# Kernel tuning notes

Measured on AMD Instinct MI355X. Metric: run time of the kernel, lower is better.

## Reference

```python
import jax, jax.numpy as jnp
import numpy as np

B, L, D = 4096, 50, 64
NU, NI, NR = 100000, 100000, 5


def setup_inputs() -> dict:
    key = jax.random.key(0)
    ks = jax.random.split(key, 16)
    s = 0.02
    inp = {
        "nodes_v": jax.random.randint(ks[0], (B,), 0, NI),
        "neigh_u": jax.random.randint(ks[1], (B, L), 0, NU),
        "neigh_r": jax.random.randint(ks[2], (B, L), 0, NR),
        "embed_u": jax.random.normal(ks[3], (NU, D)) * s,
        "embed_i": jax.random.normal(ks[4], (NI, D)) * s,
        "embed_r": jax.random.normal(ks[5], (NR, D)) * s,
        # gv MLP: Linear(2D,D) ReLU Linear(D,D) ReLU Linear(D,D)
        "gv_w1": jax.random.normal(ks[6], (2 * D, D)) * s, "gv_b1": jnp.zeros((D,)),
        "gv_w2": jax.random.normal(ks[7], (D, D)) * s,     "gv_b2": jnp.zeros((D,)),
        "gv_w3": jax.random.normal(ks[8], (D, D)) * s,     "gv_b3": jnp.zeros((D,)),
        # attention MLP: Linear(2D,D) ReLU Linear(D,D) ReLU Linear(D,1), softmax over neighbors
        "att_w1": jax.random.normal(ks[9], (2 * D, D)) * s, "att_b1": jnp.zeros((D,)),
        "att_w2": jax.random.normal(ks[10], (D, D)) * s,    "att_b2": jnp.zeros((D,)),
        "att_w3": jax.random.normal(ks[11], (D, 1)) * s,    "att_b3": jnp.zeros((1,)),
        # combine: Linear(2D,D) ReLU Linear(D,D) ReLU
        "wr1_w": jax.random.normal(ks[12], (2 * D, D)) * s, "wr1_b": jnp.zeros((D,)),
        "wr2_w": jax.random.normal(ks[13], (D, D)) * s,     "wr2_b": jnp.zeros((D,)),
    }
    return inp


def reference(nodes_v, neigh_u, neigh_r, embed_u, embed_i, embed_r,
              gv_w1, gv_b1, gv_w2, gv_b2, gv_w3, gv_b3,
              att_w1, att_b1, att_w2, att_b2, att_w3, att_b3,
              wr1_w, wr1_b, wr2_w, wr2_b):
    qj = embed_i[nodes_v]            # [B, D] item reps
    pt = embed_u[neigh_u]            # [B, L, D] neighbor user reps
    er = embed_r[neigh_r]            # [B, L, D] rating reps
    # fusion MLP g(.)
    x = jnp.concatenate([pt, er], axis=-1)                    # [B, L, 2D]
    h = jax.nn.relu(x @ gv_w1 + gv_b1)
    h = jax.nn.relu(h @ gv_w2 + gv_b2)
    fjt = h @ gv_w3 + gv_b3                                   # [B, L, D]
    # attention over neighbors (dropout is identity in eval mode)
    q_rep = jnp.broadcast_to(qj[:, None, :], fjt.shape)       # [B, L, D]
    a = jnp.concatenate([fjt, q_rep], axis=-1)                # [B, L, 2D]
    a = jax.nn.relu(a @ att_w1 + att_b1)
    a = jax.nn.relu(a @ att_w2 + att_b2)
    scores = (a @ att_w3 + att_b3)[..., 0]                    # [B, L]
    mu = jax.nn.softmax(scores, axis=1)                       # softmax over neighbors
    zj = jnp.einsum("bld,bl->bd", fjt, mu)                   # weighted aggregation
    # combine aggregated neighborhood with item's own embedding (2D -> D)
    z = jax.nn.relu(jnp.concatenate([zj, qj], axis=-1) @ wr1_w + wr1_b)
    out = jax.nn.relu(z @ wr2_w + wr2_b)                      # [B, D]
    return out
```

## Files before the change

kernel.cpp:

```cpp
#include <hip/hip_runtime.h>

typedef __bf16 bf16;
typedef short s16x8 __attribute__((ext_vector_type(8)));
typedef __bf16 b16x8 __attribute__((ext_vector_type(8)));
typedef float f32x4 __attribute__((ext_vector_type(4)));

#define B_   4096
#define L_   50
#define SH   72

#define OFF_W1F  0
#define OFF_W2F  8192
#define OFF_W3F  12288
#define OFF_WCF  16384
#define OFF_A2F  20480
#define OFF_R1T  24576
#define OFF_R2T  32768
#define WT_TOTAL 36864
#define BIAS1P_BYTE 73728
#define CQ_BYTE     73984
#define EU16_BYTE   1122560
#define ER16_BYTE   13922560
#define WS_NEED     13923200

#define PREP_W_BLOCKS 145
#define CQ_BLOCKS     32
#define CONV_THREADS  800040
#define CONV_BLOCKS   3126

__device__ __forceinline__ unsigned short f2b(float f) {
    __bf16 h = (__bf16)f;
    return __builtin_bit_cast(unsigned short, h);
}
__device__ __forceinline__ unsigned pack2(float a, float b) {
    return (unsigned)f2b(a) | ((unsigned)f2b(b) << 16);
}
__device__ __forceinline__ s16x8 mkfrag(float4 a, float4 b) {
    union { s16x8 v; unsigned u[4]; } r;
    r.u[0] = pack2(a.x, a.y); r.u[1] = pack2(a.z, a.w);
    r.u[2] = pack2(b.x, b.y); r.u[3] = pack2(b.z, b.w);
    return r.v;
}
__device__ __forceinline__ f32x4 mfma16(s16x8 a, s16x8 b, f32x4 c) {
    return __builtin_amdgcn_mfma_f32_16x16x32_bf16(a, b, c, 0, 0, 0);
}

extern "C" __global__ void prep_all(const float* __restrict__ w1, const float* __restrict__ w2,
                                    const float* __restrict__ w3, const float* __restrict__ a1,
                                    const float* __restrict__ a2, const float* __restrict__ r1,
                                    const float* __restrict__ r2, const float* __restrict__ gb3,
                                    const float* __restrict__ ab1,
                                    const int* __restrict__ nodes_v, const float* __restrict__ embed_i,
                                    const float* __restrict__ embed_u, const float* __restrict__ embed_r,
                                    bf16* __restrict__ wt, float* __restrict__ bias1p,
                                    float* __restrict__ cq,
                                    bf16* __restrict__ eu16, bf16* __restrict__ er16)
{
    if (blockIdx.x >= PREP_W_BLOCKS + CQ_BLOCKS) {
        long t = (long)(blockIdx.x - PREP_W_BLOCKS - CQ_BLOCKS) * 256 + threadIdx.x;
        if (t < 800000) {
            const float* s = embed_u + t * 8;
            float4 a = *(const float4*)s, b = *(const float4*)(s + 4);
            *(s16x8*)(eu16 + t * 8) = mkfrag(a, b);
        } else if (t < CONV_THREADS) {
            long r = (t - 800000) * 8;
            const float* s = embed_r + r;
            float4 a = *(const float4*)s, b = *(const float4*)(s + 4);
            *(s16x8*)(er16 + r) = mkfrag(a, b);
        }
        return;
    }
    if (blockIdx.x >= PREP_W_BLOCKS) {
        int wv   = (blockIdx.x - PREP_W_BLOCKS) * 4 + (threadIdx.x >> 6);
        int lane = threadIdx.x & 63, m = lane & 15, quad = lane >> 4;
        int base = wv * 32;
        int i0 = base + m, i1 = base + 16 + m;
        int v0 = nodes_v[i0], v1 = nodes_v[i1];

        s16x8 bfr[8];
#pragma unroll
        for (int kt = 0; kt < 2; ++kt)
#pragma unroll
            for (int nt = 0; nt < 4; ++nt) {
                const float* src = a1 + (64 + kt * 32 + quad * 8) * 64 + nt * 16 + m;
                union { s16x8 v; unsigned u[4]; } fr;
#pragma unroll
                for (int jj = 0; jj < 4; ++jj)
                    fr.u[jj] = pack2(src[(2 * jj) * 64], src[(2 * jj + 1) * 64]);
                bfr[kt * 4 + nt] = fr.v;
            }

        f32x4 ac0[4] = {}, ac1[4] = {};
#pragma unroll
        for (int kt = 0; kt < 2; ++kt) {
            const float* q0 = embed_i + (size_t)v0 * 64 + kt * 32 + quad * 8;
            const float* q1 = embed_i + (size_t)v1 * 64 + kt * 32 + quad * 8;
            s16x8 aq0 = mkfrag(*(const float4*)q0, *(const float4*)(q0 + 4));
            s16x8 aq1 = mkfrag(*(const float4*)q1, *(const float4*)(q1 + 4));
#pragma unroll
            for (int nt = 0; nt < 4; ++nt) {
                ac0[nt] = mfma16(aq0, bfr[kt * 4 + nt], ac0[nt]);
                ac1[nt] = mfma16(aq1, bfr[kt * 4 + nt], ac1[nt]);
            }
        }
#pragma unroll
        for (int nt = 0; nt < 4; ++nt) {
            int c = nt * 16 + m;
#pragma unroll
            for (int r4 = 0; r4 < 4; ++r4) {
                cq[(base + quad * 4 + r4) * 64 + c]      = ac0[nt][r4];
                cq[(base + 16 + quad * 4 + r4) * 64 + c] = ac1[nt][r4];
            }
        }
        return;
    }
    int i = blockIdx.x * 256 + threadIdx.x;
    if (i >= WT_TOTAL + 64) return;
    if (i >= WT_TOTAL) {
        int n = i - WT_TOTAL;
        float s0 = ab1[n], s1 = 0.f, s2 = 0.f, s3 = 0.f;
#pragma unroll
        for (int t = 0; t < 64; t += 4) {
            s0 = fmaf(gb3[t],     a1[t * 64 + n],       s0);
            s1 = fmaf(gb3[t + 1], a1[(t + 1) * 64 + n], s1);
            s2 = fmaf(gb3[t + 2], a1[(t + 2) * 64 + n], s2);
            s3 = fmaf(gb3[t + 3], a1[(t + 3) * 64 + n], s3);
        }
        bias1p[n] = (s0 + s1) + (s2 + s3);
        return;
    }
    float val;
    if (i < OFF_R1T) {
        int off, kind;
        if      (i < OFF_W2F) { off = OFF_W1F; kind = 0; }
        else if (i < OFF_W3F) { off = OFF_W2F; kind = 1; }
        else if (i < OFF_WCF) { off = OFF_W3F; kind = 2; }
        else if (i < OFF_A2F) { off = OFF_WCF; kind = 3; }
        else                  { off = OFF_A2F; kind = 4; }
        int local = i - off;
        int f = local >> 9, lane = (local >> 3) & 63, j = local & 7;
        int kt = f >> 2, nt = f & 3, quad = lane >> 4, m = lane & 15;
        int k = kt * 32 + quad * 8 + j;
        int n = nt * 16 + m;
        if (kind == 0)      val = w1[k * 64 + n];
        else if (kind == 1) val = w2[k * 64 + n];
        else if (kind == 2) val = w3[k * 64 + n];
        else if (kind == 4) val = a2[k * 64 + n];
        else {
            float s0 = 0.f, s1 = 0.f, s2 = 0.f, s3 = 0.f;
#pragma unroll
            for (int t = 0; t < 64; t += 4) {
                float4 w = *(const float4*)(w3 + k * 64 + t);
                s0 = fmaf(w.x, a1[t * 64 + n],       s0);
                s1 = fmaf(w.y, a1[(t + 1) * 64 + n], s1);
                s2 = fmaf(w.z, a1[(t + 2) * 64 + n], s2);
                s3 = fmaf(w.w, a1[(t + 3) * 64 + n], s3);
            }
            val = (s0 + s1) + (s2 + s3);
        }
    }
    else if (i < OFF_R2T) { int li = i - OFF_R1T; int n = li >> 7, k = li & 127; val = r1[k * 64 + n]; }
    else                  { int li = i - OFF_R2T; int n = li >> 6, k = li & 63;  val = r2[k * 64 + n]; }
    wt[i] = (bf16)val;
}

template<bool BF16E>
__global__ void __launch_bounds__(256, 2)
dense_fused(const int* __restrict__ nodes_v, const int* __restrict__ neigh_u,
            const int* __restrict__ neigh_r,
            const float* __restrict__ embed_u, const float* __restrict__ embed_i,
            const float* __restrict__ embed_r,
            const float* __restrict__ gv_b1, const float* __restrict__ gv_b2,
            const float* __restrict__ gv_b3,
            const float* __restrict__ att_b2, const float* __restrict__ att_w3,
            const float* __restrict__ wr1_b, const float* __restrict__ wr2_b,
            const bf16* __restrict__ wt, const bf16* __restrict__ eu16,
            const bf16* __restrict__ er16, const float* __restrict__ cq,
            const float* __restrict__ bias1p, float* __restrict__ out)
{
    __shared__ __align__(16) bf16 H[128 * SH];
    __shared__ float zp[4 * 64];
    __shared__ float swm[4 * 2];
    __shared__ float qsh[2 * 64];

    const int tid = threadIdx.x;
    const int lane = tid & 63, wave = tid >> 6;
    const int m = lane & 15, quad = lane >> 4;
    const int b0 = blockIdx.x * 2;
    const int rw0 = wave * 32;
    const int item_w = rw0 >> 6;
    const int lbase = rw0 & 63;

    const int bw = b0 + item_w;
    const int l0 = min(lbase + m, L_ - 1);
    const int l1 = min(lbase + 16 + m, L_ - 1);
    const int u0 = neigh_u[bw * L_ + l0], u1 = neigh_u[bw * L_ + l1];
    const int v0 = neigh_r[bw * L_ + l0], v1 = neigh_r[bw * L_ + l1];

    float cs4[4];
#pragma unroll
    for (int nt = 0; nt < 4; ++nt) {
        int c = nt * 16 + m;
        cs4[nt] = cq[bw * 64 + c] + bias1p[c];
    }

    bf16* Hw = H + rw0 * SH;
    bf16* H0 = Hw;
    bf16* H1 = Hw + 16 * SH;

    {
        f32x4 ac0[4] = {}, ac1[4] = {};
        if constexpr (BF16E) {
            const bf16* p00 = eu16 + (size_t)u0 * 64;
            const bf16* p01 = eu16 + (size_t)u1 * 64;
            const bf16* p10 = er16 + v0 * 64;
            const bf16* p11 = er16 + v1 * 64;
#pragma unroll
            for (int kt = 0; kt < 4; ++kt) {
                const bf16* s0p = (kt < 2 ? p00 : p10) + (kt & 1) * 32 + quad * 8;
                const bf16* s1p = (kt < 2 ? p01 : p11) + (kt & 1) * 32 + quad * 8;
                s16x8 a0 = *(const s16x8*)s0p;
                s16x8 a1 = *(const s16x8*)s1p;
#pragma unroll
                for (int nt = 0; nt < 4; ++nt) {
                    s16x8 bfr = *(const s16x8*)(wt + OFF_W1F + (kt * 4 + nt) * 512 + lane * 8);
                    ac0[nt] = mfma16(a0, bfr, ac0[nt]);
                    ac1[nt] = mfma16(a1, bfr, ac1[nt]);
                }
            }
        } else {
            const float* b00 = embed_u + (size_t)u0 * 64;
            const float* b01 = embed_u + (size_t)u1 * 64;
            const float* b10 = embed_r + v0 * 64;
            const float* b11 = embed_r + v1 * 64;
#pragma unroll
            for (int kt = 0; kt < 4; ++kt) {
                const float* s0p = (kt < 2 ? b00 : b10) + (kt & 1) * 32 + quad * 8;
                const float* s1p = (kt < 2 ? b01 : b11) + (kt & 1) * 32 + quad * 8;
                float4 a0a = *(const float4*)s0p, a0b = *(const float4*)(s0p + 4);
                float4 a1a = *(const float4*)s1p, a1b = *(const float4*)(s1p + 4);
                s16x8 a0 = mkfrag(a0a, a0b);
                s16x8 a1 = mkfrag(a1a, a1b);
#pragma unroll
                for (int nt = 0; nt < 4; ++nt) {
                    s16x8 bfr = *(const s16x8*)(wt + OFF_W1F + (kt * 4 + nt) * 512 + lane * 8);
                    ac0[nt] = mfma16(a0, bfr, ac0[nt]);
                    ac1[nt] = mfma16(a1, bfr, ac1[nt]);
                }
            }
        }
#pragma unroll
        for (int nt = 0; nt < 4; ++nt) {
            int c = nt * 16 + m;
            float bv = gv_b1[c];
#pragma unroll
            for (int r4 = 0; r4 < 4; ++r4) {
                H0[(quad * 4 + r4) * SH + c] = (bf16)fmaxf(ac0[nt][r4] + bv, 0.f);
                H1[(quad * 4 + r4) * SH + c] = (bf16)fmaxf(ac1[nt][r4] + bv, 0.f);
            }
        }
    }

    {
        f32x4 ac0[4] = {}, ac1[4] = {};
#pragma unroll
        for (int kt = 0; kt < 2; ++kt) {
            s16x8 a0 = *(const s16x8*)(H0 + m * SH + kt * 32 + quad * 8);
            s16x8 a1 = *(const s16x8*)(H1 + m * SH + kt * 32 + quad * 8);
#pragma unroll
            for (int nt = 0; nt < 4; ++nt) {
                s16x8 bfr = *(const s16x8*)(wt + OFF_W2F + (kt * 4 + nt) * 512 + lane * 8);
                ac0[nt] = mfma16(a0, bfr, ac0[nt]);
                ac1[nt] = mfma16(a1, bfr, ac1[nt]);
            }
        }
#pragma unroll
        for (int nt = 0; nt < 4; ++nt) {
            int c = nt * 16 + m;
            float bv = gv_b2[c];
#pragma unroll
            for (int r4 = 0; r4 < 4; ++r4) {
                H0[(quad * 4 + r4) * SH + c] = (bf16)fmaxf(ac0[nt][r4] + bv, 0.f);
                H1[(quad * 4 + r4) * SH + c] = (bf16)fmaxf(ac1[nt][r4] + bv, 0.f);
            }
        }
    }

    f32x4 aF0[4] = {}, aF1[4] = {};
    {
        f32x4 aA0[4] = {}, aA1[4] = {};
#pragma unroll
        for (int kt = 0; kt < 2; ++kt) {
            s16x8 a0 = *(const s16x8*)(H0 + m * SH + kt * 32 + quad * 8);
            s16x8 a1 = *(const s16x8*)(H1 + m * SH + kt * 32 + quad * 8);
#pragma unroll
            for (int nt = 0; nt < 4; ++nt) {
                s16x8 bF = *(const s16x8*)(wt + OFF_W3F + (kt * 4 + nt) * 512 + lane * 8);
                s16x8 bA = *(const s16x8*)(wt + OFF_WCF + (kt * 4 + nt) * 512 + lane * 8);
                aF0[nt] = mfma16(a0, bF, aF0[nt]);
                aF1[nt] = mfma16(a1, bF, aF1[nt]);
                aA0[nt] = mfma16(a0, bA, aA0[nt]);
                aA1[nt] = mfma16(a1, bA, aA1[nt]);
            }
        }
#pragma unroll
        for (int nt = 0; nt < 4; ++nt) {
            int c = nt * 16 + m;
#pragma unroll
            for (int r4 = 0; r4 < 4; ++r4) {
                H0[(quad * 4 + r4) * SH + c] = (bf16)fmaxf(aA0[nt][r4] + cs4[nt], 0.f);
                H1[(quad * 4 + r4) * SH + c] = (bf16)fmaxf(aA1[nt][r4] + cs4[nt], 0.f);
            }
        }
    }

    float s0[4], s1[4];
    {
        f32x4 ac0[4] = {}, ac1[4] = {};
#pragma unroll
        for (int kt = 0; kt < 2; ++kt) {
            s16x8 a0 = *(const s16x8*)(H0 + m * SH + kt * 32 + quad * 8);
            s16x8 a1 = *(const s16x8*)(H1 + m * SH + kt * 32 + quad * 8);
#pragma unroll
            for (int nt = 0; nt < 4; ++nt) {
                s16x8 bfr = *(const s16x8*)(wt + OFF_A2F + (kt * 4 + nt) * 512 + lane * 8);
                ac0[nt] = mfma16(a0, bfr, ac0[nt]);
                ac1[nt] = mfma16(a1, bfr, ac1[nt]);
            }
        }
#pragma unroll
        for (int r4 = 0; r4 < 4; ++r4) { s0[r4] = 0.f; s1[r4] = 0.f; }
#pragma unroll
        for (int nt = 0; nt < 4; ++nt) {
            int c = nt * 16 + m;
            float b2v = att_b2[c], w3v = att_w3[c];
#pragma unroll
            for (int r4 = 0; r4 < 4; ++r4) {
                s0[r4] += fmaxf(ac0[nt][r4] + b2v, 0.f) * w3v;
                s1[r4] += fmaxf(ac1[nt][r4] + b2v, 0.f) * w3v;
            }
        }
#pragma unroll
        for (int mask = 1; mask < 16; mask <<= 1)
#pragma unroll
            for (int r4 = 0; r4 < 4; ++r4) {
                s0[r4] += __shfl_xor(s0[r4], mask);
                s1[r4] += __shfl_xor(s1[r4], mask);
            }
    }

    {
        const int r0b = lbase + quad * 4;
        float mloc = -1e30f;
#pragma unroll
        for (int r4 = 0; r4 < 4; ++r4) {
            if (r0b + r4 < L_)      mloc = fmaxf(mloc, s0[r4]);
            if (r0b + 16 + r4 < L_) mloc = fmaxf(mloc, s1[r4]);
        }
        mloc = fmaxf(mloc, __shfl_xor(mloc, 16));
        mloc = fmaxf(mloc, __shfl_xor(mloc, 32));

        float e0[4], e1[4], ssum = 0.f;
#pragma unroll
        for (int r4 = 0; r4 < 4; ++r4) {
            e0[r4] = (r0b + r4 < L_)      ? __expf(s0[r4] - mloc) : 0.f;
            e1[r4] = (r0b + 16 + r4 < L_) ? __expf(s1[r4] - mloc) : 0.f;
            ssum += e0[r4] + e1[r4];
        }
        ssum += __shfl_xor(ssum, 16);
        ssum += __shfl_xor(ssum, 32);

        float z[4] = {0.f, 0.f, 0.f, 0.f};
#pragma unroll
        for (int r4 = 0; r4 < 4; ++r4)
#pragma unroll
            for (int nt = 0; nt < 4; ++nt)
                z[nt] += aF0[nt][r4] * e0[r4] + aF1[nt][r4] * e1[r4];
#pragma unroll
        for (int nt = 0; nt < 4; ++nt) {
            z[nt] += __shfl_xor(z[nt], 16);
            z[nt] += __shfl_xor(z[nt], 32);
        }
        if (quad == 0) {
#pragma unroll
            for (int nt = 0; nt < 4; ++nt) zp[wave * 64 + nt * 16 + m] = z[nt];
        }
        if (lane == 0) { swm[wave * 2] = ssum; swm[wave * 2 + 1] = mloc; }
    }
    __syncthreads();

    if ((wave & 1) == 0) {
        const int item = wave >> 1;
        const int d = lane;
        float ma = swm[wave * 2 + 1],      mb = swm[(wave + 1) * 2 + 1];
        float sa = swm[wave * 2],          sb = swm[(wave + 1) * 2];
        float M  = fmaxf(ma, mb);
        float fa = __expf(ma - M), fb = __expf(mb - M);
        float zj = (fa * zp[wave * 64 + d] + fb * zp[(wave + 1) * 64 + d])
                 / (fa * sa + fb * sb) + gv_b3[d];

        float* zsh = zp + wave * 64;
        zsh[d] = zj;
        qsh[item * 64 + d] = embed_i[nodes_v[b0 + item] * 64 + d];

        float accz = wr1_b[d];
        const bf16* r1 = wt + OFF_R1T + d * 128;
#pragma unroll
        for (int k8 = 0; k8 < 8; ++k8) {
            b16x8 wv = *(const b16x8*)(r1 + k8 * 8);
#pragma unroll
            for (int j = 0; j < 8; ++j) accz = fmaf((float)wv[j], zsh[k8 * 8 + j], accz);
        }
#pragma unroll
        for (int k8 = 0; k8 < 8; ++k8) {
            b16x8 wv = *(const b16x8*)(r1 + 64 + k8 * 8);
#pragma unroll
            for (int j = 0; j < 8; ++j) accz = fmaf((float)wv[j], qsh[item * 64 + k8 * 8 + j], accz);
        }
        zsh[d] = fmaxf(accz, 0.f);

        float acco = wr2_b[d];
        const bf16* r2 = wt + OFF_R2T + d * 64;
#pragma unroll
        for (int k8 = 0; k8 < 8; ++k8) {
            b16x8 wv = *(const b16x8*)(r2 + k8 * 8);
#pragma unroll
            for (int j = 0; j < 8; ++j) acco = fmaf((float)wv[j], zsh[k8 * 8 + j], acco);
        }
        out[(b0 + item) * 64 + d] = fmaxf(acco, 0.f);
    }
}

extern "C" void kernel_launch(void* const* d_in, const int* in_sizes, int n_in,
                              void* d_out, int out_size, void* d_ws, size_t ws_size,
                              hipStream_t stream)
{
    const int* nodes_v = (const int*)d_in[0];
    const int* neigh_u = (const int*)d_in[1];
    const int* neigh_r = (const int*)d_in[2];
    const float* embed_u = (const float*)d_in[3];
    const float* embed_i = (const float*)d_in[4];
    const float* embed_r = (const float*)d_in[5];
    const float* gv_w1  = (const float*)d_in[6];  const float* gv_b1 = (const float*)d_in[7];
    const float* gv_w2  = (const float*)d_in[8];  const float* gv_b2 = (const float*)d_in[9];
    const float* gv_w3  = (const float*)d_in[10]; const float* gv_b3 = (const float*)d_in[11];
    const float* att_w1 = (const float*)d_in[12]; const float* att_b1 = (const float*)d_in[13];
    const float* att_w2 = (const float*)d_in[14]; const float* att_b2 = (const float*)d_in[15];
    const float* att_w3 = (const float*)d_in[16]; const float* att_b3 = (const float*)d_in[17];
    const float* wr1_w  = (const float*)d_in[18]; const float* wr1_b = (const float*)d_in[19];
    const float* wr2_w  = (const float*)d_in[20]; const float* wr2_b = (const float*)d_in[21];
    (void)att_b3;

    bf16*  wt     = (bf16*)d_ws;
    float* bias1p = (float*)((char*)d_ws + BIAS1P_BYTE);
    float* cq     = (float*)((char*)d_ws + CQ_BYTE);
    bf16*  eu16   = (bf16*)((char*)d_ws + EU16_BYTE);
    bf16*  er16   = (bf16*)((char*)d_ws + ER16_BYTE);

    const bool big = ws_size >= (size_t)WS_NEED;
    const int prep_grid = PREP_W_BLOCKS + CQ_BLOCKS + (big ? CONV_BLOCKS : 0);

    prep_all<<<prep_grid, 256, 0, stream>>>(
        gv_w1, gv_w2, gv_w3, att_w1, att_w2, wr1_w, wr2_w, gv_b3, att_b1,
        nodes_v, embed_i, embed_u, embed_r, wt, bias1p, cq, eu16, er16);

    if (big) {
        dense_fused<true><<<B_ / 2, 256, 0, stream>>>(nodes_v, neigh_u, neigh_r,
                                                      embed_u, embed_i, embed_r,
                                                      gv_b1, gv_b2, gv_b3, att_b2, att_w3,
                                                      wr1_b, wr2_b, wt, eu16, er16,
                                                      cq, bias1p, (float*)d_out);
    } else {
        dense_fused<false><<<B_ / 2, 256, 0, stream>>>(nodes_v, neigh_u, neigh_r,
                                                       embed_u, embed_i, embed_r,
                                                       gv_b1, gv_b2, gv_b3, att_b2, att_w3,
                                                       wr1_b, wr2_b, wt, eu16, er16,
                                                       cq, bias1p, (float*)d_out);
    }
}
```

Before: 159.3 us.

## Stage MLP weights in LDS, process four item pairs per block with gather prefetch

The fused kernel becomes persistent-ish: each block handles four item pairs instead of one. It copies the MFMA weight fragments into LDS once per block with global_load_lds, then reads them from LDS instead of global memory. The embedding gathers for the next pair are issued during the current pair's compute, with nontemporal loads to hide gather latency. In exchange it uses 48KB more LDS, which may reduce occupancy. It also launches only 512 blocks, which cuts parallelism on a 256-CU part.

```diff
diff --git a/kernel.cpp b/kernel.cpp
--- a/kernel.cpp
+++ b/kernel.cpp
@@ -17,6 +17,7 @@
 #define OFF_R1T  24576
 #define OFF_R2T  32768
 #define WT_TOTAL 36864
+#define WL_ELEMS 24576
 #define BIAS1P_BYTE 73728
 #define CQ_BYTE     73984
 #define EU16_BYTE   1122560
@@ -28,6 +29,9 @@
 #define CONV_THREADS  800040
 #define CONV_BLOCKS   3126
 
+#define DENSE_BLOCKS  512
+#define PAIRS_PER_BLK 4
+
 __device__ __forceinline__ unsigned short f2b(float f) {
     __bf16 h = (__bf16)f;
     return __builtin_bit_cast(unsigned short, h);
@@ -43,6 +47,9 @@
 }
 __device__ __forceinline__ f32x4 mfma16(s16x8 a, s16x8 b, f32x4 c) {
     return __builtin_amdgcn_mfma_f32_16x16x32_bf16(a, b, c, 0, 0, 0);
+}
+__device__ __forceinline__ s16x8 ntload16(const bf16* p) {
+    return __builtin_nontemporal_load((const s16x8*)p);
 }
 
 extern "C" __global__ void prep_all(const float* __restrict__ w1, const float* __restrict__ w2,
@@ -178,6 +185,7 @@
             const bf16* __restrict__ er16, const float* __restrict__ cq,
             const float* __restrict__ bias1p, float* __restrict__ out)
 {
+    __shared__ __align__(16) bf16 Wl[WL_ELEMS];
     __shared__ __align__(16) bf16 H[128 * SH];
     __shared__ float zp[4 * 64];
     __shared__ float swm[4 * 2];
@@ -186,248 +194,303 @@
     const int tid = threadIdx.x;
     const int lane = tid & 63, wave = tid >> 6;
     const int m = lane & 15, quad = lane >> 4;
-    const int b0 = blockIdx.x * 2;
     const int rw0 = wave * 32;
     const int item_w = rw0 >> 6;
     const int lbase = rw0 & 63;
 
-    const int bw = b0 + item_w;
-    const int l0 = min(lbase + m, L_ - 1);
-    const int l1 = min(lbase + 16 + m, L_ - 1);
-    const int u0 = neigh_u[bw * L_ + l0], u1 = neigh_u[bw * L_ + l1];
-    const int v0 = neigh_r[bw * L_ + l0], v1 = neigh_r[bw * L_ + l1];
-
-    float cs4[4];
-#pragma unroll
-    for (int nt = 0; nt < 4; ++nt) {
-        int c = nt * 16 + m;
-        cs4[nt] = cq[bw * 64 + c] + bias1p[c];
-    }
-
-    bf16* Hw = H + rw0 * SH;
-    bf16* H0 = Hw;
-    bf16* H1 = Hw + 16 * SH;
-
     {
-        f32x4 ac0[4] = {}, ac1[4] = {};
+        const char* gsrc = (const char*)wt;
+        char* ldst = (char*)Wl;
+#pragma unroll
+        for (int itc = 0; itc < 12; ++itc) {
+            int ch = itc * 4 + wave;
+            __builtin_amdgcn_global_load_lds(
+                (const __attribute__((address_space(1))) void*)(gsrc + ch * 1024 + lane * 16),
+                (__attribute__((address_space(3))) void*)(ldst + ch * 1024), 16, 0, 0);
+        }
+    }
+
+    float bp4[4];
+#pragma unroll
+    for (int nt = 0; nt < 4; ++nt) bp4[nt] = bias1p[nt * 16 + m];
+
+    s16x8 aC[8];
+    float cqv[4];
+    {
+        const int p = blockIdx.x * PAIRS_PER_BLK;
+        const int bw = p * 2 + item_w;
+        const int l0 = min(lbase + m, L_ - 1);
+        const int l1 = min(lbase + 16 + m, L_ - 1);
+        const int u0 = neigh_u[bw * L_ + l0], u1 = neigh_u[bw * L_ + l1];
+        const int v0 = neigh_r[bw * L_ + l0], v1 = neigh_r[bw * L_ + l1];
         if constexpr (BF16E) {
             const bf16* p00 = eu16 + (size_t)u0 * 64;
             const bf16* p01 = eu16 + (size_t)u1 * 64;
-            const bf16* p10 = er16 + v0 * 64;
-            const bf16* p11 = er16 + v1 * 64;
+            const bf16* p10 = er16 + (size_t)v0 * 64;
+            const bf16* p11 = er16 + (size_t)v1 * 64;
 #pragma unroll
             for (int kt = 0; kt < 4; ++kt) {
-                const bf16* s0p = (kt < 2 ? p00 : p10) + (kt & 1) * 32 + quad * 8;
-                const bf16* s1p = (kt < 2 ? p01 : p11) + (kt & 1) * 32 + quad * 8;
-                s16x8 a0 = *(const s16x8*)s0p;
-                s16x8 a1 = *(const s16x8*)s1p;
-#pragma unroll
-                for (int nt = 0; nt < 4; ++nt) {
-                    s16x8 bfr = *(const s16x8*)(wt + OFF_W1F + (kt * 4 + nt) * 512 + lane * 8);
-                    ac0[nt] = mfma16(a0, bfr, ac0[nt]);
-                    ac1[nt] = mfma16(a1, bfr, ac1[nt]);
-                }
+                aC[kt * 2]     = ntload16((kt < 2 ? p00 : p10) + (kt & 1) * 32 + quad * 8);
+                aC[kt * 2 + 1] = ntload16((kt < 2 ? p01 : p11) + (kt & 1) * 32 + quad * 8);
             }
         } else {
             const float* b00 = embed_u + (size_t)u0 * 64;
             const float* b01 = embed_u + (size_t)u1 * 64;
-            const float* b10 = embed_r + v0 * 64;
-            const float* b11 = embed_r + v1 * 64;
+            const float* b10 = embed_r + (size_t)v0 * 64;
+            const float* b11 = embed_r + (size_t)v1 * 64;
 #pragma unroll
             for (int kt = 0; kt < 4; ++kt) {
                 const float* s0p = (kt < 2 ? b00 : b10) + (kt & 1) * 32 + quad * 8;
                 const float* s1p = (kt < 2 ? b01 : b11) + (kt & 1) * 32 + quad * 8;
-                float4 a0a = *(const float4*)s0p, a0b = *(const float4*)(s0p + 4);
-                float4 a1a = *(const float4*)s1p, a1b = *(const float4*)(s1p + 4);
-                s16x8 a0 = mkfrag(a0a, a0b);
-                s16x8 a1 = mkfrag(a1a, a1b);
+                aC[kt * 2]     = mkfrag(*(const float4*)s0p, *(const float4*)(s0p + 4));
+                aC[kt * 2 + 1] = mkfrag(*(const float4*)s1p, *(const float4*)(s1p + 4));
+            }
+        }
+#pragma unroll
+        for (int nt = 0; nt < 4; ++nt) cqv[nt] = cq[bw * 64 + nt * 16 + m];
+    }
+
+    __syncthreads();
+
+    bf16* H0 = H + rw0 * SH;
+    bf16* H1 = H0 + 16 * SH;
+
+#pragma unroll 1
+    for (int it = 0; it < PAIRS_PER_BLK; ++it) {
+        const int p  = blockIdx.x * PAIRS_PER_BLK + it;
+        const int b0 = p * 2;
+        const int bw = b0 + item_w;
+
+        float cs4[4];
+#pragma unroll
+        for (int nt = 0; nt < 4; ++nt) cs4[nt] = cqv[nt] + bp4[nt];
+
+        {
+            f32x4 ac0[4] = {}, ac1[4] = {};
+#pragma unroll
+            for (int kt = 0; kt < 4; ++kt) {
+                s16x8 a0 = aC[kt * 2], a1 = aC[kt * 2 + 1];
 #pragma unroll
                 for (int nt = 0; nt < 4; ++nt) {
-                    s16x8 bfr = *(const s16x8*)(wt + OFF_W1F + (kt * 4 + nt) * 512 + lane * 8);
+                    s16x8 bfr = *(const s16x8*)(Wl + OFF_W1F + (kt * 4 + nt) * 512 + lane * 8);
                     ac0[nt] = mfma16(a0, bfr, ac0[nt]);
                     ac1[nt] = mfma16(a1, bfr, ac1[nt]);
                 }
             }
-        }
-#pragma unroll
-        for (int nt = 0; nt < 4; ++nt) {
-            int c = nt * 16 + m;
-            float bv = gv_b1[c];
+#pragma unroll
+            for (int nt = 0; nt < 4; ++nt) {
+                int c = nt * 16 + m;
+                float bv = gv_b1[c];
+#pragma unroll
+                for (int r4 = 0; r4 < 4; ++r4) {
+                    H0[(quad * 4 + r4) * SH + c] = (bf16)fmaxf(ac0[nt][r4] + bv, 0.f);
+                    H1[(quad * 4 + r4) * SH + c] = (bf16)fmaxf(ac1[nt][r4] + bv, 0.f);
+                }
+            }
+        }
+
+        if (it + 1 < PAIRS_PER_BLK) {
+            const int bwN = (p + 1) * 2 + item_w;
+            const int l0 = min(lbase + m, L_ - 1);
+            const int l1 = min(lbase + 16 + m, L_ - 1);
+            const int u0 = neigh_u[bwN * L_ + l0], u1 = neigh_u[bwN * L_ + l1];
+            const int v0 = neigh_r[bwN * L_ + l0], v1 = neigh_r[bwN * L_ + l1];
+            if constexpr (BF16E) {
+                const bf16* p00 = eu16 + (size_t)u0 * 64;
+                const bf16* p01 = eu16 + (size_t)u1 * 64;
+                const bf16* p10 = er16 + (size_t)v0 * 64;
+                const bf16* p11 = er16 + (size_t)v1 * 64;
+#pragma unroll
+                for (int kt = 0; kt < 4; ++kt) {
+                    aC[kt * 2]     = ntload16((kt < 2 ? p00 : p10) + (kt & 1) * 32 + quad * 8);
+                    aC[kt * 2 + 1] = ntload16((kt < 2 ? p01 : p11) + (kt & 1) * 32 + quad * 8);
+                }
+            } else {
+                const float* b00 = embed_u + (size_t)u0 * 64;
+                const float* b01 = embed_u + (size_t)u1 * 64;
+                const float* b10 = embed_r + (size_t)v0 * 64;
+                const float* b11 = embed_r + (size_t)v1 * 64;
+#pragma unroll
+                for (int kt = 0; kt < 4; ++kt) {
+                    const float* s0p = (kt < 2 ? b00 : b10) + (kt & 1) * 32 + quad * 8;
+                    const float* s1p = (kt < 2 ? b01 : b11) + (kt & 1) * 32 + quad * 8;
+                    aC[kt * 2]     = mkfrag(*(const float4*)s0p, *(const float4*)(s0p + 4));
+                    aC[kt * 2 + 1] = mkfrag(*(const float4*)s1p, *(const float4*)(s1p + 4));
+                }
+            }
+#pragma unroll
+            for (int nt = 0; nt < 4; ++nt) cqv[nt] = cq[bwN * 64 + nt * 16 + m];
+        }
+
+        {
+            f32x4 ac0[4] = {}, ac1[4] = {};
+#pragma unroll
+            for (int kt = 0; kt < 2; ++kt) {
+                s16x8 a0 = *(const s16x8*)(H0 + m * SH + kt * 32 + quad * 8);
+                s16x8 a1 = *(const s16x8*)(H1 + m * SH + kt * 32 + quad * 8);
+#pragma unroll
+                for (int nt = 0; nt < 4; ++nt) {
+                    s16x8 bfr = *(const s16x8*)(Wl + OFF_W2F + (kt * 4 + nt) * 512 + lane * 8);
+                    ac0[nt] = mfma16(a0, bfr, ac0[nt]);
+                    ac1[nt] = mfma16(a1, bfr, ac1[nt]);
+                }
+            }
+#pragma unroll
+            for (int nt = 0; nt < 4; ++nt) {
+                int c = nt * 16 + m;
+                float bv = gv_b2[c];
+#pragma unroll
+                for (int r4 = 0; r4 < 4; ++r4) {
+                    H0[(quad * 4 + r4) * SH + c] = (bf16)fmaxf(ac0[nt][r4] + bv, 0.f);
+                    H1[(quad * 4 + r4) * SH + c] = (bf16)fmaxf(ac1[nt][r4] + bv, 0.f);
+                }
+            }
+        }
+
+        f32x4 aF0[4] = {}, aF1[4] = {};
+        {
+            f32x4 aA0[4] = {}, aA1[4] = {};
+#pragma unroll
+            for (int kt = 0; kt < 2; ++kt) {
+                s16x8 a0 = *(const s16x8*)(H0 + m * SH + kt * 32 + quad * 8);
+                s16x8 a1 = *(const s16x8*)(H1 + m * SH + kt * 32 + quad * 8);
+#pragma unroll
+                for (int nt = 0; nt < 4; ++nt) {
+                    s16x8 bF = *(const s16x8*)(Wl + OFF_W3F + (kt * 4 + nt) * 512 + lane * 8);
+                    s16x8 bA = *(const s16x8*)(Wl + OFF_WCF + (kt * 4 + nt) * 512 + lane * 8);
+                    aF0[nt] = mfma16(a0, bF, aF0[nt]);
+                    aF1[nt] = mfma16(a1, bF, aF1[nt]);
+                    aA0[nt] = mfma16(a0, bA, aA0[nt]);
+                    aA1[nt] = mfma16(a1, bA, aA1[nt]);
+                }
+            }
+#pragma unroll
+            for (int nt = 0; nt < 4; ++nt) {
+                int c = nt * 16 + m;
+#pragma unroll
+                for (int r4 = 0; r4 < 4; ++r4) {
+                    H0[(quad * 4 + r4) * SH + c] = (bf16)fmaxf(aA0[nt][r4] + cs4[nt], 0.f);
+                    H1[(quad * 4 + r4) * SH + c] = (bf16)fmaxf(aA1[nt][r4] + cs4[nt], 0.f);
+                }
+            }
+        }
+
+        float s0[4], s1[4];
+        {
+            f32x4 ac0[4] = {}, ac1[4] = {};
+#pragma unroll
+            for (int kt = 0; kt < 2; ++kt) {
+                s16x8 a0 = *(const s16x8*)(H0 + m * SH + kt * 32 + quad * 8);
+                s16x8 a1 = *(const s16x8*)(H1 + m * SH + kt * 32 + quad * 8);
+#pragma unroll
+                for (int nt = 0; nt < 4; ++nt) {
+                    s16x8 bfr = *(const s16x8*)(Wl + OFF_A2F + (kt * 4 + nt) * 512 + lane * 8);
+                    ac0[nt] = mfma16(a0, bfr, ac0[nt]);
+                    ac1[nt] = mfma16(a1, bfr, ac1[nt]);
+                }
+            }
+#pragma unroll
+            for (int r4 = 0; r4 < 4; ++r4) { s0[r4] = 0.f; s1[r4] = 0.f; }
+#pragma unroll
+            for (int nt = 0; nt < 4; ++nt) {
+                int c = nt * 16 + m;
+                float b2v = att_b2[c], w3v = att_w3[c];
+#pragma unroll
+                for (int r4 = 0; r4 < 4; ++r4) {
+                    s0[r4] += fmaxf(ac0[nt][r4] + b2v, 0.f) * w3v;
+                    s1[r4] += fmaxf(ac1[nt][r4] + b2v, 0.f) * w3v;
+                }
+            }
+#pragma unroll
+            for (int mask = 1; mask < 16; mask <<= 1)
+#pragma unroll
+                for (int r4 = 0; r4 < 4; ++r4) {
+                    s0[r4] += __shfl_xor(s0[r4], mask);
+                    s1[r4] += __shfl_xor(s1[r4], mask);
+                }
+        }
+
+        {
+            const int r0b = lbase + quad * 4;
+            float mloc = -1e30f;
 #pragma unroll
             for (int r4 = 0; r4 < 4; ++r4) {
-                H0[(quad * 4 + r4) * SH + c] = (bf16)fmaxf(ac0[nt][r4] + bv, 0.f);
-                H1[(quad * 4 + r4) * SH + c] = (bf16)fmaxf(ac1[nt][r4] + bv, 0.f);
-            }
-        }
-    }
-
-    {
-        f32x4 ac0[4] = {}, ac1[4] = {};
-#pragma unroll
-        for (int kt = 0; kt < 2; ++kt) {
-            s16x8 a0 = *(const s16x8*)(H0 + m * SH + kt * 32 + quad * 8);
-            s16x8 a1 = *(const s16x8*)(H1 + m * SH + kt * 32 + quad * 8);
-#pragma unroll
-            for (int nt = 0; nt < 4; ++nt) {
-                s16x8 bfr = *(const s16x8*)(wt + OFF_W2F + (kt * 4 + nt) * 512 + lane * 8);
-                ac0[nt] = mfma16(a0, bfr, ac0[nt]);
-                ac1[nt] = mfma16(a1, bfr, ac1[nt]);
-            }
-        }
-#pragma unroll
-        for (int nt = 0; nt < 4; ++nt) {
-            int c = nt * 16 + m;
-            float bv = gv_b2[c];
+                if (r0b + r4 < L_)      mloc = fmaxf(mloc, s0[r4]);
+                if (r0b + 16 + r4 < L_) mloc = fmaxf(mloc, s1[r4]);
+            }
+            mloc = fmaxf(mloc, __shfl_xor(mloc, 16));
+            mloc = fmaxf(mloc, __shfl_xor(mloc, 32));
+
+            float e0[4], e1[4], ssum = 0.f;
 #pragma unroll
             for (int r4 = 0; r4 < 4; ++r4) {
-                H0[(quad * 4 + r4) * SH + c] = (bf16)fmaxf(ac0[nt][r4] + bv, 0.f);
-                H1[(quad * 4 + r4) * SH + c] = (bf16)fmaxf(ac1[nt][r4] + bv, 0.f);
-            }
-        }
-    }
-
-    f32x4 aF0[4] = {}, aF1[4] = {};
-    {
-        f32x4 aA0[4] = {}, aA1[4] = {};
-#pragma unroll
-        for (int kt = 0; kt < 2; ++kt) {
-            s16x8 a0 = *(const s16x8*)(H0 + m * SH + kt * 32 + quad * 8);
-            s16x8 a1 = *(const s16x8*)(H1 + m * SH + kt * 32 + quad * 8);
-#pragma unroll
-            for (int nt = 0; nt < 4; ++nt) {
-                s16x8 bF = *(const s16x8*)(wt + OFF_W3F + (kt * 4 + nt) * 512 + lane * 8);
-                s16x8 bA = *(const s16x8*)(wt + OFF_WCF + (kt * 4 + nt) * 512 + lane * 8);
-                aF0[nt] = mfma16(a0, bF, aF0[nt]);
-                aF1[nt] = mfma16(a1, bF, aF1[nt]);
-                aA0[nt] = mfma16(a0, bA, aA0[nt]);
-                aA1[nt] = mfma16(a1, bA, aA1[nt]);
-            }
-        }
-#pragma unroll
-        for (int nt = 0; nt < 4; ++nt) {
-            int c = nt * 16 + m;
-#pragma unroll
-            for (int r4 = 0; r4 < 4; ++r4) {
-                H0[(quad * 4 + r4) * SH + c] = (bf16)fmaxf(aA0[nt][r4] + cs4[nt], 0.f);
-                H1[(quad * 4 + r4) * SH + c] = (bf16)fmaxf(aA1[nt][r4] + cs4[nt], 0.f);
-            }
-        }
-    }
-
-    float s0[4], s1[4];
-    {
-        f32x4 ac0[4] = {}, ac1[4] = {};
-#pragma unroll
-        for (int kt = 0; kt < 2; ++kt) {
-            s16x8 a0 = *(const s16x8*)(H0 + m * SH + kt * 32 + quad * 8);
-            s16x8 a1 = *(const s16x8*)(H1 + m * SH + kt * 32 + quad * 8);
-#pragma unroll
-            for (int nt = 0; nt < 4; ++nt) {
-                s16x8 bfr = *(const s16x8*)(wt + OFF_A2F + (kt * 4 + nt) * 512 + lane * 8);
-                ac0[nt] = mfma16(a0, bfr, ac0[nt]);
-                ac1[nt] = mfma16(a1, bfr, ac1[nt]);
-            }
-        }
-#pragma unroll
-        for (int r4 = 0; r4 < 4; ++r4) { s0[r4] = 0.f; s1[r4] = 0.f; }
-#pragma unroll
-        for (int nt = 0; nt < 4; ++nt) {
-            int c = nt * 16 + m;
-            float b2v = att_b2[c], w3v = att_w3[c];
-#pragma unroll
-            for (int r4 = 0; r4 < 4; ++r4) {
-                s0[r4] += fmaxf(ac0[nt][r4] + b2v, 0.f) * w3v;
-                s1[r4] += fmaxf(ac1[nt][r4] + b2v, 0.f) * w3v;
-            }
-        }
-#pragma unroll
-        for (int mask = 1; mask < 16; mask <<= 1)
-#pragma unroll
-            for (int r4 = 0; r4 < 4; ++r4) {
-                s0[r4] += __shfl_xor(s0[r4], mask);
-                s1[r4] += __shfl_xor(s1[r4], mask);
-            }
-    }
-
-    {
-        const int r0b = lbase + quad * 4;
-        float mloc = -1e30f;
-#pragma unroll
-        for (int r4 = 0; r4 < 4; ++r4) {
-            if (r0b + r4 < L_)      mloc = fmaxf(mloc, s0[r4]);
-            if (r0b + 16 + r4 < L_) mloc = fmaxf(mloc, s1[r4]);
-        }
-        mloc = fmaxf(mloc, __shfl_xor(mloc, 16));
-        mloc = fmaxf(mloc, __shfl_xor(mloc, 32));
-
-        float e0[4], e1[4], ssum = 0.f;
-#pragma unroll
-        for (int r4 = 0; r4 < 4; ++r4) {
-            e0[r4] = (r0b + r4 < L_)      ? __expf(s0[r4] - mloc) : 0.f;
-            e1[r4] = (r0b + 16 + r4 < L_) ? __expf(s1[r4] - mloc) : 0.f;
-            ssum += e0[r4] + e1[r4];
-        }
-        ssum += __shfl_xor(ssum, 16);
-        ssum += __shfl_xor(ssum, 32);
-
-        float z[4] = {0.f, 0.f, 0.f, 0.f};
-#pragma unroll
-        for (int r4 = 0; r4 < 4; ++r4)
-#pragma unroll
-            for (int nt = 0; nt < 4; ++nt)
-                z[nt] += aF0[nt][r4] * e0[r4] + aF1[nt][r4] * e1[r4];
-#pragma unroll
-        for (int nt = 0; nt < 4; ++nt) {
-            z[nt] += __shfl_xor(z[nt], 16);
-            z[nt] += __shfl_xor(z[nt], 32);
-        }
-        if (quad == 0) {
-#pragma unroll
-            for (int nt = 0; nt < 4; ++nt) zp[wave * 64 + nt * 16 + m] = z[nt];
-        }
-        if (lane == 0) { swm[wave * 2] = ssum; swm[wave * 2 + 1] = mloc; }
-    }
-    __syncthreads();
-
-    if ((wave & 1) == 0) {
-        const int item = wave >> 1;
-        const int d = lane;
-        float ma = swm[wave * 2 + 1],      mb = swm[(wave + 1) * 2 + 1];
-        float sa = swm[wave * 2],          sb = swm[(wave + 1) * 2];
-        float M  = fmaxf(ma, mb);
-        float fa = __expf(ma - M), fb = __expf(mb - M);
-        float zj = (fa * zp[wave * 64 + d] + fb * zp[(wave + 1) * 64 + d])
-                 / (fa * sa + fb * sb) + gv_b3[d];
-
-        float* zsh = zp + wave * 64;
-        zsh[d] = zj;
-        qsh[item * 64 + d] = embed_i[nodes_v[b0 + item] * 64 + d];
-
-        float accz = wr1_b[d];
-        const bf16* r1 = wt + OFF_R1T + d * 128;
-#pragma unroll
-        for (int k8 = 0; k8 < 8; ++k8) {
-            b16x8 wv = *(const b16x8*)(r1 + k8 * 8);
-#pragma unroll
-            for (int j = 0; j < 8; ++j) accz = fmaf((float)wv[j], zsh[k8 * 8 + j], accz);
-        }
-#pragma unroll
-        for (int k8 = 0; k8 < 8; ++k8) {
-            b16x8 wv = *(const b16x8*)(r1 + 64 + k8 * 8);
-#pragma unroll
-            for (int j = 0; j < 8; ++j) accz = fmaf((float)wv[j], qsh[item * 64 + k8 * 8 + j], accz);
-        }
-        zsh[d] = fmaxf(accz, 0.f);
-
-        float acco = wr2_b[d];
-        const bf16* r2 = wt + OFF_R2T + d * 64;
-#pragma unroll
-        for (int k8 = 0; k8 < 8; ++k8) {
-            b16x8 wv = *(const b16x8*)(r2 + k8 * 8);
-#pragma unroll
-            for (int j = 0; j < 8; ++j) acco = fmaf((float)wv[j], zsh[k8 * 8 + j], acco);
-        }
-        out[(b0 + item) * 64 + d] = fmaxf(acco, 0.f);
+                e0[r4] = (r0b + r4 < L_)      ? __expf(s0[r4] - mloc) : 0.f;
+                e1[r4] = (r0b + 16 + r4 < L_) ? __expf(s1[r4] - mloc) : 0.f;
+                ssum += e0[r4] + e1[r4];
+            }
+            ssum += __shfl_xor(ssum, 16);
+            ssum += __shfl_xor(ssum, 32);
+
+            float z[4] = {0.f, 0.f, 0.f, 0.f};
+#pragma unroll
+            for (int r4 = 0; r4 < 4; ++r4)
+#pragma unroll
+                for (int nt = 0; nt < 4; ++nt)
+                    z[nt] += aF0[nt][r4] * e0[r4] + aF1[nt][r4] * e1[r4];
+#pragma unroll
+            for (int nt = 0; nt < 4; ++nt) {
+                z[nt] += __shfl_xor(z[nt], 16);
+                z[nt] += __shfl_xor(z[nt], 32);
+            }
+            if (quad == 0) {
+#pragma unroll
+                for (int nt = 0; nt < 4; ++nt) zp[wave * 64 + nt * 16 + m] = z[nt];
+            }
+            if (lane == 0) { swm[wave * 2] = ssum; swm[wave * 2 + 1] = mloc; }
+        }
+        __syncthreads();
+
+        if ((wave & 1) == 0) {
+            const int item = wave >> 1;
+            const int d = lane;
+            float ma = swm[wave * 2 + 1],      mb = swm[(wave + 1) * 2 + 1];
+            float sa = swm[wave * 2],          sb = swm[(wave + 1) * 2];
+            float M  = fmaxf(ma, mb);
+            float fa = __expf(ma - M), fb = __expf(mb - M);
+            float zj = (fa * zp[wave * 64 + d] + fb * zp[(wave + 1) * 64 + d])
+                     / (fa * sa + fb * sb) + gv_b3[d];
+
+            float* zsh = zp + wave * 64;
+            zsh[d] = zj;
+            qsh[item * 64 + d] = embed_i[(size_t)nodes_v[b0 + item] * 64 + d];
+
+            float accz = wr1_b[d];
+            const bf16* r1 = wt + OFF_R1T + d * 128;
+#pragma unroll
+            for (int k8 = 0; k8 < 8; ++k8) {
+                b16x8 wv = *(const b16x8*)(r1 + k8 * 8);
+#pragma unroll
+                for (int j = 0; j < 8; ++j) accz = fmaf((float)wv[j], zsh[k8 * 8 + j], accz);
+            }
+#pragma unroll
+            for (int k8 = 0; k8 < 8; ++k8) {
+                b16x8 wv = *(const b16x8*)(r1 + 64 + k8 * 8);
+#pragma unroll
+                for (int j = 0; j < 8; ++j) accz = fmaf((float)wv[j], qsh[item * 64 + k8 * 8 + j], accz);
+            }
+            zsh[d] = fmaxf(accz, 0.f);
+
+            float acco = wr2_b[d];
+            const bf16* r2 = wt + OFF_R2T + d * 64;
+#pragma unroll
+            for (int k8 = 0; k8 < 8; ++k8) {
+                b16x8 wv = *(const b16x8*)(r2 + k8 * 8);
+#pragma unroll
+                for (int j = 0; j < 8; ++j) acco = fmaf((float)wv[j], zsh[k8 * 8 + j], acco);
+            }
+            out[(size_t)(b0 + item) * 64 + d] = fmaxf(acco, 0.f);
+        }
+        __syncthreads();
     }
 }
 
@@ -465,16 +528,16 @@
         nodes_v, embed_i, embed_u, embed_r, wt, bias1p, cq, eu16, er16);
 
     if (big) {
-        dense_fused<true><<<B_ / 2, 256, 0, stream>>>(nodes_v, neigh_u, neigh_r,
-                                                      embed_u, embed_i, embed_r,
-                                                      gv_b1, gv_b2, gv_b3, att_b2, att_w3,
-                                                      wr1_b, wr2_b, wt, eu16, er16,
-                                                      cq, bias1p, (float*)d_out);
+        dense_fused<true><<<DENSE_BLOCKS, 256, 0, stream>>>(nodes_v, neigh_u, neigh_r,
+                                                            embed_u, embed_i, embed_r,
+                                                            gv_b1, gv_b2, gv_b3, att_b2, att_w3,
+                                                            wr1_b, wr2_b, wt, eu16, er16,
+                                                            cq, bias1p, (float*)d_out);
     } else {
-        dense_fused<false><<<B_ / 2, 256, 0, stream>>>(nodes_v, neigh_u, neigh_r,
-                                                       embed_u, embed_i, embed_r,
-                                                       gv_b1, gv_b2, gv_b3, att_b2, att_w3,
-                                                       wr1_b, wr2_b, wt, eu16, er16,
-                                                       cq, bias1p, (float*)d_out);
-    }
-}
+        dense_fused<false><<<DENSE_BLOCKS, 256, 0, stream>>>(nodes_v, neigh_u, neigh_r,
+                                                             embed_u, embed_i, embed_r,
+                                                             gv_b1, gv_b2, gv_b3, att_b2, att_w3,
+                                                             wr1_b, wr2_b, wt, eu16, er16,
+                                                             cq, bias1p, (float*)d_out);
+    }
+}
```

New measurement: 160.8 us. Within noise of the previous version (+0.9%).

## Store hidden activations transposed in LDS and read via ds_read_b64_tr_b16

Applied to the files above, without the earlier changes.

Intermediate MLP activations were written to LDS as scalar bf16 stores into a padded row-major tile and read back as row fragments. They are now packed two-per-word into 8-byte stores in a transposed per-wave layout, and read back with the gfx950 transpose-load instruction ds_read_b64_tr_b16 through inline asm. The aim is fewer LDS store instructions and fewer bank conflicts between MFMA layers. The gathered bf16 embedding rows now use nontemporal loads, and some index arithmetic is widened to size_t. The risk is a hand-written asm sequence with an explicit waitcnt and sched_barrier, which limits how well the compiler can overlap these reads with other work.

```diff
diff --git a/kernel.cpp b/kernel.cpp
--- a/kernel.cpp
+++ b/kernel.cpp
@@ -4,10 +4,10 @@
 typedef short s16x8 __attribute__((ext_vector_type(8)));
 typedef __bf16 b16x8 __attribute__((ext_vector_type(8)));
 typedef float f32x4 __attribute__((ext_vector_type(4)));
+typedef unsigned u32x2 __attribute__((ext_vector_type(2)));
 
 #define B_   4096
 #define L_   50
-#define SH   72
 
 #define OFF_W1F  0
 #define OFF_W2F  8192
@@ -43,6 +43,9 @@
 }
 __device__ __forceinline__ f32x4 mfma16(s16x8 a, s16x8 b, f32x4 c) {
     return __builtin_amdgcn_mfma_f32_16x16x32_bf16(a, b, c, 0, 0, 0);
+}
+__device__ __forceinline__ s16x8 ntload16(const bf16* p) {
+    return __builtin_nontemporal_load((const s16x8*)p);
 }
 
 extern "C" __global__ void prep_all(const float* __restrict__ w1, const float* __restrict__ w2,
@@ -178,7 +181,7 @@
             const bf16* __restrict__ er16, const float* __restrict__ cq,
             const float* __restrict__ bias1p, float* __restrict__ out)
 {
-    __shared__ __align__(16) bf16 H[128 * SH];
+    __shared__ __align__(16) bf16 Ht[4 * 2048];
     __shared__ float zp[4 * 64];
     __shared__ float swm[4 * 2];
     __shared__ float qsh[2 * 64];
@@ -191,6 +194,50 @@
     const int item_w = rw0 >> 6;
     const int lbase = rw0 & 63;
 
+    bf16* HT0 = Ht + wave * 2048;
+    bf16* HT1 = HT0 + 1024;
+    bf16* st0 = HT0 + m * 16 + quad * 4;
+    bf16* st1 = HT1 + m * 16 + quad * 4;
+    const __attribute__((address_space(3))) bf16* rd0 =
+        (const __attribute__((address_space(3))) bf16*)(HT0 + quad * 128 + m);
+    const __attribute__((address_space(3))) bf16* rd1 =
+        (const __attribute__((address_space(3))) bf16*)(HT1 + quad * 128 + m);
+
+#define HT_STORE(stp, vals, bias_expr)                                            \
+    {                                                                             \
+        _Pragma("unroll")                                                         \
+        for (int nt = 0; nt < 4; ++nt) {                                          \
+            float b_ = bias_expr;                                                 \
+            u32x2 w_;                                                             \
+            w_.x = pack2(fmaxf(vals[nt][0] + b_, 0.f), fmaxf(vals[nt][1] + b_, 0.f)); \
+            w_.y = pack2(fmaxf(vals[nt][2] + b_, 0.f), fmaxf(vals[nt][3] + b_, 0.f)); \
+            *(u32x2*)((stp) + nt * 256) = w_;                                     \
+        }                                                                         \
+    }
+
+#define HT_READ8(q0,q1,q2,q3,p0,p1,p2,p3)                                         \
+    asm volatile("ds_read_b64_tr_b16 %0, %4\n\t"                                  \
+                 "ds_read_b64_tr_b16 %1, %4 offset:128\n\t"                       \
+                 "ds_read_b64_tr_b16 %2, %4 offset:1024\n\t"                      \
+                 "ds_read_b64_tr_b16 %3, %4 offset:1152"                          \
+                 : "=&v"(q0), "=&v"(q1), "=&v"(q2), "=&v"(q3)                     \
+                 : "v"(rd0) : "memory");                                          \
+    asm volatile("ds_read_b64_tr_b16 %0, %4\n\t"                                  \
+                 "ds_read_b64_tr_b16 %1, %4 offset:128\n\t"                       \
+                 "ds_read_b64_tr_b16 %2, %4 offset:1024\n\t"                      \
+                 "ds_read_b64_tr_b16 %3, %4 offset:1152"                          \
+                 : "=&v"(p0), "=&v"(p1), "=&v"(p2), "=&v"(p3)                     \
+                 : "v"(rd1) : "memory");                                          \
+    asm volatile("s_waitcnt lgkmcnt(0)" ::: "memory");                            \
+    __builtin_amdgcn_sched_barrier(0)
+
+#define ASM_FRAGS(A00,A01,A10,A11,q0,q1,q2,q3,p0,p1,p2,p3)                        \
+    union { s16x8 v; u32x2 u[2]; } A00, A01, A10, A11;                            \
+    A00.u[0] = q0; A00.u[1] = q1;                                  \
+    A01.u[0] = q2; A01.u[1] = q3;                                  \
+    A10.u[0] = p0; A10.u[1] = p1;                                  \
+    A11.u[0] = p2; A11.u[1] = p3
+
     const int bw = b0 + item_w;
     const int l0 = min(lbase + m, L_ - 1);
     const int l1 = min(lbase + 16 + m, L_ - 1);
@@ -204,23 +251,17 @@
         cs4[nt] = cq[bw * 64 + c] + bias1p[c];
     }
 
-    bf16* Hw = H + rw0 * SH;
-    bf16* H0 = Hw;
-    bf16* H1 = Hw + 16 * SH;
-
     {
         f32x4 ac0[4] = {}, ac1[4] = {};
         if constexpr (BF16E) {
             const bf16* p00 = eu16 + (size_t)u0 * 64;
             const bf16* p01 = eu16 + (size_t)u1 * 64;
-            const bf16* p10 = er16 + v0 * 64;
-            const bf16* p11 = er16 + v1 * 64;
+            const bf16* p10 = er16 + (size_t)v0 * 64;
+            const bf16* p11 = er16 + (size_t)v1 * 64;
 #pragma unroll
             for (int kt = 0; kt < 4; ++kt) {
-                const bf16* s0p = (kt < 2 ? p00 : p10) + (kt & 1) * 32 + quad * 8;
-                const bf16* s1p = (kt < 2 ? p01 : p11) + (kt & 1) * 32 + quad * 8;
-                s16x8 a0 = *(const s16x8*)s0p;
-                s16x8 a1 = *(const s16x8*)s1p;
+                s16x8 a0 = ntload16((kt < 2 ? p00 : p10) + (kt & 1) * 32 + quad * 8);
+                s16x8 a1 = ntload16((kt < 2 ? p01 : p11) + (kt & 1) * 32 + quad * 8);
 #pragma unroll
                 for (int nt = 0; nt < 4; ++nt) {
                     s16x8 bfr = *(const s16x8*)(wt + OFF_W1F + (kt * 4 + nt) * 512 + lane * 8);
@@ -231,16 +272,14 @@
         } else {
             const float* b00 = embed_u + (size_t)u0 * 64;
             const float* b01 = embed_u + (size_t)u1 * 64;
-            const float* b10 = embed_r + v0 * 64;
-            const float* b11 = embed_r + v1 * 64;
+            const float* b10 = embed_r + (size_t)v0 * 64;
+            const float* b11 = embed_r + (size_t)v1 * 64;
 #pragma unroll
             for (int kt = 0; kt < 4; ++kt) {
                 const float* s0p = (kt < 2 ? b00 : b10) + (kt & 1) * 32 + quad * 8;
                 const float* s1p = (kt < 2 ? b01 : b11) + (kt & 1) * 32 + quad * 8;
-                float4 a0a = *(const float4*)s0p, a0b = *(const float4*)(s0p + 4);
-                float4 a1a = *(const float4*)s1p, a1b = *(const float4*)(s1p + 4);
-                s16x8 a0 = mkfrag(a0a, a0b);
-                s16x8 a1 = mkfrag(a1a, a1b);
+                s16x8 a0 = mkfrag(*(const float4*)s0p, *(const float4*)(s0p + 4));
+                s16x8 a1 = mkfrag(*(const float4*)s1p, *(const float4*)(s1p + 4));
 #pragma unroll
                 for (int nt = 0; nt < 4; ++nt) {
                     s16x8 bfr = *(const s16x8*)(wt + OFF_W1F + (kt * 4 + nt) * 512 + lane * 8);
@@ -249,24 +288,19 @@
                 }
             }
         }
-#pragma unroll
-        for (int nt = 0; nt < 4; ++nt) {
-            int c = nt * 16 + m;
-            float bv = gv_b1[c];
-#pragma unroll
-            for (int r4 = 0; r4 < 4; ++r4) {
-                H0[(quad * 4 + r4) * SH + c] = (bf16)fmaxf(ac0[nt][r4] + bv, 0.f);
-                H1[(quad * 4 + r4) * SH + c] = (bf16)fmaxf(ac1[nt][r4] + bv, 0.f);
-            }
-        }
+        HT_STORE(st0, ac0, gv_b1[nt * 16 + m]);
+        HT_STORE(st1, ac1, gv_b1[nt * 16 + m]);
     }
 
     {
+        u32x2 q0, q1, q2, q3, p0, p1, p2, p3;
+        HT_READ8(q0, q1, q2, q3, p0, p1, p2, p3);
+        ASM_FRAGS(A00, A01, A10, A11, q0, q1, q2, q3, p0, p1, p2, p3);
         f32x4 ac0[4] = {}, ac1[4] = {};
 #pragma unroll
         for (int kt = 0; kt < 2; ++kt) {
-            s16x8 a0 = *(const s16x8*)(H0 + m * SH + kt * 32 + quad * 8);
-            s16x8 a1 = *(const s16x8*)(H1 + m * SH + kt * 32 + quad * 8);
+            s16x8 a0 = kt ? A01.v : A00.v;
+            s16x8 a1 = kt ? A11.v : A10.v;
 #pragma unroll
             for (int nt = 0; nt < 4; ++nt) {
                 s16x8 bfr = *(const s16x8*)(wt + OFF_W2F + (kt * 4 + nt) * 512 + lane * 8);
@@ -274,25 +308,20 @@
                 ac1[nt] = mfma16(a1, bfr, ac1[nt]);
             }
         }
-#pragma unroll
-        for (int nt = 0; nt < 4; ++nt) {
-            int c = nt * 16 + m;
-            float bv = gv_b2[c];
-#pragma unroll
-            for (int r4 = 0; r4 < 4; ++r4) {
-                H0[(quad * 4 + r4) * SH + c] = (bf16)fmaxf(ac0[nt][r4] + bv, 0.f);
-                H1[(quad * 4 + r4) * SH + c] = (bf16)fmaxf(ac1[nt][r4] + bv, 0.f);
-            }
-        }
+        HT_STORE(st0, ac0, gv_b2[nt * 16 + m]);
+        HT_STORE(st1, ac1, gv_b2[nt * 16 + m]);
     }
 
     f32x4 aF0[4] = {}, aF1[4] = {};
     {
+        u32x2 q0, q1, q2, q3, p0, p1, p2, p3;
+        HT_READ8(q0, q1, q2, q3, p0, p1, p2, p3);
+        ASM_FRAGS(A00, A01, A10, A11, q0, q1, q2, q3, p0, p1, p2, p3);
         f32x4 aA0[4] = {}, aA1[4] = {};
 #pragma unroll
         for (int kt = 0; kt < 2; ++kt) {
-            s16x8 a0 = *(const s16x8*)(H0 + m * SH + kt * 32 + quad * 8);
-            s16x8 a1 = *(const s16x8*)(H1 + m * SH + kt * 32 + quad * 8);
+            s16x8 a0 = kt ? A01.v : A00.v;
+            s16x8 a1 = kt ? A11.v : A10.v;
 #pragma unroll
             for (int nt = 0; nt < 4; ++nt) {
                 s16x8 bF = *(const s16x8*)(wt + OFF_W3F + (kt * 4 + nt) * 512 + lane * 8);
@@ -303,24 +332,20 @@
                 aA1[nt] = mfma16(a1, bA, aA1[nt]);
             }
         }
-#pragma unroll
-        for (int nt = 0; nt < 4; ++nt) {
-            int c = nt * 16 + m;
-#pragma unroll
-            for (int r4 = 0; r4 < 4; ++r4) {
-                H0[(quad * 4 + r4) * SH + c] = (bf16)fmaxf(aA0[nt][r4] + cs4[nt], 0.f);
-                H1[(quad * 4 + r4) * SH + c] = (bf16)fmaxf(aA1[nt][r4] + cs4[nt], 0.f);
-            }
-        }
+        HT_STORE(st0, aA0, cs4[nt]);
+        HT_STORE(st1, aA1, cs4[nt]);
     }
 
     float s0[4], s1[4];
     {
+        u32x2 q0, q1, q2, q3, p0, p1, p2, p3;
+        HT_READ8(q0, q1, q2, q3, p0, p1, p2, p3);
+        ASM_FRAGS(A00, A01, A10, A11, q0, q1, q2, q3, p0, p1, p2, p3);
         f32x4 ac0[4] = {}, ac1[4] = {};
 #pragma unroll
         for (int kt = 0; kt < 2; ++kt) {
-            s16x8 a0 = *(const s16x8*)(H0 + m * SH + kt * 32 + quad * 8);
-            s16x8 a1 = *(const s16x8*)(H1 + m * SH + kt * 32 + quad * 8);
+            s16x8 a0 = kt ? A01.v : A00.v;
+            s16x8 a1 = kt ? A11.v : A10.v;
 #pragma unroll
             for (int nt = 0; nt < 4; ++nt) {
                 s16x8 bfr = *(const s16x8*)(wt + OFF_A2F + (kt * 4 + nt) * 512 + lane * 8);
@@ -401,7 +426,7 @@
 
         float* zsh = zp + wave * 64;
         zsh[d] = zj;
-        qsh[item * 64 + d] = embed_i[nodes_v[b0 + item] * 64 + d];
+        qsh[item * 64 + d] = embed_i[(size_t)nodes_v[b0 + item] * 64 + d];
 
         float accz = wr1_b[d];
         const bf16* r1 = wt + OFF_R1T + d * 128;
@@ -427,8 +452,11 @@
 #pragma unroll
             for (int j = 0; j < 8; ++j) acco = fmaf((float)wv[j], zsh[k8 * 8 + j], acco);
         }
-        out[(b0 + item) * 64 + d] = fmaxf(acco, 0.f);
-    }
+        out[(size_t)(b0 + item) * 64 + d] = fmaxf(acco, 0.f);
+    }
+#undef HT_STORE
+#undef HT_READ8
+#undef ASM_FRAGS
 }
 
 extern "C" void kernel_launch(void* const* d_in, const int* in_sizes, int n_in,
```

New measurement: 164.9 us. 3.5% more time.
